# Performance work log

Measured on AMD Instinct MI355X. Metric: run time of the kernel, lower is better.

Reference implementation:

```python
import jax, jax.numpy as jnp
import numpy as np

EPS = 1e-13


def _masked_softmax(logits, mask_last):
    # logits: [B, Q, K]; mask_last: [B, 1, K] float {0,1}
    # Faithful to torch source: multiply logits by mask (NOT additive -inf),
    # softmax, re-mask, renormalize.
    p = jax.nn.softmax(logits * mask_last, axis=-1) * mask_last
    return p / (jnp.sum(p, axis=-1, keepdims=True) + EPS)


def setup_inputs() -> dict:
    key = jax.random.key(0)
    k1, k2, k3, k4 = jax.random.split(key, 4)
    B, LA, LB, H = 16, 1024, 1024, 512
    premise_batch = jax.random.normal(k1, (B, LA, H), dtype=jnp.float32)
    hypothesis_batch = jax.random.normal(k2, (B, LB, H), dtype=jnp.float32)
    premise_mask = jax.random.randint(k3, (B, LA), 0, 2).astype(jnp.float32)
    hypothesis_mask = jax.random.randint(k4, (B, LB), 0, 2).astype(jnp.float32)
    # avoid fully-masked rows (degenerate)
    premise_mask = premise_mask.at[:, 0].set(1.0)
    hypothesis_mask = hypothesis_mask.at[:, 0].set(1.0)
    return {
        "premise_batch": premise_batch,
        "premise_mask": premise_mask,
        "hypothesis_batch": hypothesis_batch,
        "hypothesis_mask": hypothesis_mask,
    }


def reference(premise_batch, premise_mask, hypothesis_batch, hypothesis_mask):
    # sim[b,i,j] = <a_i, b_j>
    sim = jnp.einsum("bih,bjh->bij", premise_batch, hypothesis_batch)
    prem_hyp_attn = _masked_softmax(sim, hypothesis_mask[:, None, :])           # [B,LA,LB]
    hyp_prem_attn = _masked_softmax(sim.transpose(0, 2, 1), premise_mask[:, None, :])  # [B,LB,LA]
    attended_premises = jnp.einsum("bij,bjh->bih", prem_hyp_attn, hypothesis_batch)
    attended_premises = attended_premises * premise_mask[:, :, None]
    attended_hypotheses = jnp.einsum("bji,bjh->bih", hyp_prem_attn.transpose(0, 2, 1), premise_batch)
    attended_hypotheses = attended_hypotheses * hypothesis_mask[:, :, None]
    return (attended_premises, attended_hypotheses)
```

## Files before the change

### kernel.cpp

```cpp
#include <hip/hip_runtime.h>
#include <hip/hip_fp16.h>
#include <math.h>

#define NB   16
#define SLA  1024
#define SLB  1024
#define HH   512

typedef __attribute__((ext_vector_type(4))) float  f32x4;
typedef __attribute__((ext_vector_type(8))) short  s16x8;
typedef __attribute__((ext_vector_type(4))) int    i32x4;

#define QS    (6.5f / 127.f)
#define QINVS (127.f / 6.5f)

__device__ __forceinline__ unsigned short f2bf(float x){
  unsigned u = __float_as_uint(x);
  u += 0x7fffu + ((u >> 16) & 1u);
  return (unsigned short)(u >> 16);
}
__device__ __forceinline__ float bf2f(unsigned short h){
  return __uint_as_float(((unsigned)h) << 16);
}
__device__ __forceinline__ float h2f(unsigned short h){
  return __half2float(__ushort_as_half(h));
}
__device__ __forceinline__ unsigned fkey(float f){
  unsigned u = __float_as_uint(f);
  return ((int)u < 0) ? ~u : (u | 0x80000000u);
}
__device__ __forceinline__ float funkey(unsigned k){
  return __uint_as_float((k & 0x80000000u) ? (k & 0x7fffffffu) : ~k);
}

__device__ __forceinline__ void gl2lds16(const void* g, void* l){
  __builtin_amdgcn_global_load_lds(
      (__attribute__((address_space(1))) unsigned int*)(unsigned long long)(size_t)g,
      (__attribute__((address_space(3))) unsigned int*)(unsigned int)(size_t)l,
      16, 0, 0);
}

__global__ __launch_bounds__(256) void scan_kernel(
    const float* __restrict__ pmask, const float* __restrict__ hmask,
    int* __restrict__ pIdx, int* __restrict__ hIdx,
    int* __restrict__ pCnt, int* __restrict__ hCnt,
    int* __restrict__ pPad, int* __restrict__ hPad,
    unsigned* __restrict__ rowMaxU, unsigned* __restrict__ colMaxU)
{
  __shared__ int ps[256];
  const int b     = blockIdx.x;
  const int which = blockIdx.y;
  const int t     = threadIdx.x;
  const float* m = (which ? hmask : pmask) + b * 1024;
  int* idx = (which ? hIdx : pIdx) + b * 1024;
  int* cnt = which ? hCnt : pCnt;
  int* pad = which ? hPad : pPad;

  #pragma unroll
  for (int v = 0; v < 4; ++v){
    int g = b * 1024 + t + v * 256;
    if (which == 0){
      rowMaxU[g] = 0u;
    } else {
      colMaxU[g] = 0u;
    }
  }

  int f[4], s = 0;
  #pragma unroll
  for (int e = 0; e < 4; ++e){
    f[e] = m[t * 4 + e] > 0.5f ? 1 : 0;
    s += f[e];
  }
  ps[t] = s;
  __syncthreads();
  for (int off = 1; off < 256; off <<= 1){
    int v = (t >= off) ? ps[t - off] : 0;
    __syncthreads();
    ps[t] += v;
    __syncthreads();
  }
  int pos = ps[t] - s;
  #pragma unroll
  for (int e = 0; e < 4; ++e){
    if (f[e]) idx[pos++] = t * 4 + e;
  }
  if (t == 0){
    int total = ps[255];
    cnt[b] = total;
    pad[b] = (total + 127) & ~127;
  }
}

__global__ __launch_bounds__(256) void zero_out_kernel(
    const float* __restrict__ pmask, const float* __restrict__ hmask,
    float* __restrict__ out)
{
  const int r = blockIdx.x * 4 + (threadIdx.x >> 6);
  const int side = r >> 14;
  const int b    = (r >> 10) & 15;
  const int row  = r & 1023;
  const float mv = (side ? hmask : pmask)[b * 1024 + row];
  if (mv > 0.5f) return;
  float4 z = {0.f, 0.f, 0.f, 0.f};
  float* p = out + (size_t)side * NB * SLA * HH
                 + ((size_t)b * 1024 + row) * 512 + (threadIdx.x & 63) * 8;
  *(float4*)p = z;
  *(float4*)(p + 4) = z;
}

__global__ __launch_bounds__(256) void cvt_gather_kernel(
    const float* __restrict__ prem, const float* __restrict__ hyp,
    const int* __restrict__ pIdx, const int* __restrict__ hIdx,
    const int* __restrict__ pCnt, const int* __restrict__ hCnt,
    const int* __restrict__ pPad, const int* __restrict__ hPad,
    char* __restrict__ premD1, char* __restrict__ premD0,
    char* __restrict__ hypD1,  char* __restrict__ hypD0,
    unsigned short* __restrict__ PremT, unsigned short* __restrict__ HypT)
{
  __shared__ unsigned short tv[64][72];
  __shared__ int sIdx[64];

  const int tensor = blockIdx.z >> 4;
  const int b  = blockIdx.z & 15;
  const int l0 = blockIdx.y * 64;
  const int h0 = blockIdx.x * 64;
  const int t  = threadIdx.x;

  const int cnt = tensor ? hCnt[b] : pCnt[b];
  const int pad = tensor ? hPad[b] : pPad[b];
  if (l0 >= pad) return;

  const float* X = tensor ? hyp : prem;
  const int* idx = (tensor ? hIdx : pIdx) + b * 1024;
  char* D1 = tensor ? hypD1 : premD1;
  char* D0 = tensor ? hypD0 : premD0;
  unsigned short* XT = tensor ? HypT : PremT;

  if (t < 64){
    int jc = l0 + t;
    sIdx[t] = (jc < cnt) ? idx[jc] : -1;
  }
  __syncthreads();

  #pragma unroll
  for (int it = 0; it < 4; ++it){
    int r = (t >> 4) + it * 16;
    int c = (t & 15) * 4;
    int orig = sIdx[r];
    float4 x = {0.f, 0.f, 0.f, 0.f};
    if (orig >= 0)
      x = *(const float4*)(X + ((size_t)b * 1024 + orig) * HH + h0 + c);
    float xv[4] = {x.x, x.y, x.z, x.w};
    char d1v[4], d0v[4];
    #pragma unroll
    for (int e = 0; e < 4; ++e){
      float xs = xv[e] * QINVS;
      float x1 = rintf(xs);
      x1 = fminf(127.f, fmaxf(-127.f, x1));
      float x0 = rintf((xs - x1) * 256.f);
      x0 = fminf(127.f, fmaxf(-128.f, x0));
      d1v[e] = (char)(int)x1;
      d0v[e] = (char)(int)x0;
      tv[c + e][r] = f2bf(xv[e]);
    }
    size_t go = ((size_t)b * 1024 + l0 + r) * HH + h0 + c;
    *(char4*)(D1 + go) = make_char4(d1v[0], d1v[1], d1v[2], d1v[3]);
    *(char4*)(D0 + go) = make_char4(d0v[0], d0v[1], d0v[2], d0v[3]);
  }
  __syncthreads();
  const int w   = t >> 2;
  const int seg = (t & 3) * 16;
  const uint4* src = (const uint4*)&tv[w][seg];
  uint4* dst = (uint4*)(XT + ((size_t)b * HH + h0 + w) * 1024 + l0 + seg);
  dst[0] = src[0];
  dst[1] = src[1];
}

__global__ __launch_bounds__(256, 3) void sim_gemm_v6_kernel(
    const char* __restrict__ premD1, const char* __restrict__ premD0,
    const char* __restrict__ hypD1,  const char* __restrict__ hypD0,
    const int* __restrict__ pCnt, const int* __restrict__ hCnt,
    const int* __restrict__ pPad, const int* __restrict__ hPad,
    unsigned short* __restrict__ simH, unsigned short* __restrict__ simT,
    unsigned* __restrict__ rowMaxU, unsigned* __restrict__ colMaxU)
{
  union __align__(16) Smem {
    struct {
      char A1[128 * 64];
      char A0[128 * 64];
      char B1[64 * 64];
      char B0[64 * 64];
    } g;
    unsigned short tp[64][136];
  };
  __shared__ Smem su;
#define sA1 (su.g.A1)
#define sA0 (su.g.A0)
#define sB1 (su.g.B1)
#define sB0 (su.g.B0)

  const int b  = blockIdx.z;
  const int i0 = blockIdx.y * 128;
  const int j0 = blockIdx.x * 64;
  const int t  = threadIdx.x;

  const int pc = pCnt[b], hc = hCnt[b];
  if (i0 >= pPad[b] || j0 >= hPad[b]) return;

  const char* A1 = premD1 + ((size_t)b * 1024 + i0) * HH;
  const char* A0 = premD0 + ((size_t)b * 1024 + i0) * HH;
  const char* B1 = hypD1  + ((size_t)b * 1024 + j0) * HH;
  const char* B0 = hypD0  + ((size_t)b * 1024 + j0) * HH;

  const int sr = t >> 2;
  const int gc = ((t & 3) ^ (sr & 3)) * 16;
  const int lco = (t & 3) * 16;

  const int lane = t & 63;
  const int wr = (t >> 7) & 1;
  const int wc = (t >> 6) & 1;
  const int q  = lane >> 4;
  const int ln = lane & 15;
  const int fo = (q ^ (ln & 3)) * 16;

  i32x4 acc1[4][2], accc[4][2];
  #pragma unroll
  for (int mt = 0; mt < 4; ++mt)
    #pragma unroll
    for (int nt = 0; nt < 2; ++nt){
      acc1[mt][nt] = (i32x4){0, 0, 0, 0};
      accc[mt][nt] = (i32x4){0, 0, 0, 0};
    }

  for (int k0 = 0; k0 < HH; k0 += 64){
    __syncthreads();
    {
      const size_t goA = (size_t)sr * HH + k0 + gc;
      gl2lds16(A1 + goA, &sA1[sr * 64 + lco]);
      gl2lds16(A0 + goA, &sA0[sr * 64 + lco]);
      const size_t goA2 = (size_t)(64 + sr) * HH + k0 + gc;
      gl2lds16(A1 + goA2, &sA1[(64 + sr) * 64 + lco]);
      gl2lds16(A0 + goA2, &sA0[(64 + sr) * 64 + lco]);
      gl2lds16(B1 + goA, &sB1[sr * 64 + lco]);
      gl2lds16(B0 + goA, &sB0[sr * 64 + lco]);
    }
    __syncthreads();

    i32x4 af[4], bf1[2], bf0[2];
    #pragma unroll
    for (int mt = 0; mt < 4; ++mt)
      af[mt] = *(const i32x4*)&sA1[(wr * 64 + mt * 16 + ln) * 64 + fo];
    #pragma unroll
    for (int nt = 0; nt < 2; ++nt)
      bf1[nt] = *(const i32x4*)&sB1[(wc * 32 + nt * 16 + ln) * 64 + fo];
    #pragma unroll
    for (int mt = 0; mt < 4; ++mt)
      #pragma unroll
      for (int nt = 0; nt < 2; ++nt)
        acc1[mt][nt] = __builtin_amdgcn_mfma_i32_16x16x64_i8(af[mt], bf1[nt], acc1[mt][nt], 0, 0, 0);
    #pragma unroll
    for (int nt = 0; nt < 2; ++nt)
      bf0[nt] = *(const i32x4*)&sB0[(wc * 32 + nt * 16 + ln) * 64 + fo];
    #pragma unroll
    for (int mt = 0; mt < 4; ++mt)
      #pragma unroll
      for (int nt = 0; nt < 2; ++nt)
        accc[mt][nt] = __builtin_amdgcn_mfma_i32_16x16x64_i8(af[mt], bf0[nt], accc[mt][nt], 0, 0, 0);
    #pragma unroll
    for (int mt = 0; mt < 4; ++mt)
      af[mt] = *(const i32x4*)&sA0[(wr * 64 + mt * 16 + ln) * 64 + fo];
    #pragma unroll
    for (int mt = 0; mt < 4; ++mt)
      #pragma unroll
      for (int nt = 0; nt < 2; ++nt)
        accc[mt][nt] = __builtin_amdgcn_mfma_i32_16x16x64_i8(af[mt], bf1[nt], accc[mt][nt], 0, 0, 0);
  }

  const float S2 = QS * QS;
  unsigned short* simb = simH + ((size_t)b * SLA + i0) * SLB + j0;

  float rmx[16];
  #pragma unroll
  for (int e = 0; e < 16; ++e) rmx[e] = -1e30f;
  float cmx[2];
  cmx[0] = -1e30f; cmx[1] = -1e30f;

  __syncthreads();

  #pragma unroll
  for (int mt = 0; mt < 4; ++mt){
    #pragma unroll
    for (int nt = 0; nt < 2; ++nt){
      int col = wc * 32 + nt * 16 + ln;
      bool colv = (j0 + col) < hc;
      unsigned short hv[4];
      #pragma unroll
      for (int rr = 0; rr < 4; ++rr){
        int row = wr * 64 + mt * 16 + q * 4 + rr;
        float f = S2 * ((float)acc1[mt][nt][rr] + (float)accc[mt][nt][rr] * 0.00390625f);
        unsigned short hb = __half_as_ushort(__float2half(f));
        simb[(size_t)row * SLB + col] = hb;
        hv[rr] = hb;
        rmx[mt * 4 + rr] = fmaxf(rmx[mt * 4 + rr], colv ? f : -1e30f);
        cmx[nt] = fmaxf(cmx[nt], (i0 + row) < pc ? f : -1e30f);
      }
      uint2 w;
      w.x = (unsigned)hv[0] | ((unsigned)hv[1] << 16);
      w.y = (unsigned)hv[2] | ((unsigned)hv[3] << 16);
      *(uint2*)&su.tp[col][wr * 64 + mt * 16 + q * 4] = w;
    }
  }
  __syncthreads();
  {
    const int jr  = t >> 2;
    const int seg = (t & 3) * 32;
    const uint4* src = (const uint4*)&su.tp[jr][seg];
    uint4* dst = (uint4*)(simT + ((size_t)b * SLB + j0 + jr) * SLA + i0 + seg);
    dst[0] = src[0];
    dst[1] = src[1];
    dst[2] = src[2];
    dst[3] = src[3];
  }

  #pragma unroll
  for (int e = 0; e < 16; ++e){
    float v = rmx[e];
    v = fmaxf(v, __shfl_xor(v, 1));
    v = fmaxf(v, __shfl_xor(v, 2));
    v = fmaxf(v, __shfl_xor(v, 4));
    v = fmaxf(v, __shfl_xor(v, 8));
    if (ln == 0){
      int row = wr * 64 + (e >> 2) * 16 + q * 4 + (e & 3);
      if (i0 + row < pc)
        atomicMax(rowMaxU + b * 1024 + i0 + row, fkey(v));
    }
  }
  #pragma unroll
  for (int nt = 0; nt < 2; ++nt){
    float v = cmx[nt];
    v = fmaxf(v, __shfl_xor(v, 16));
    v = fmaxf(v, __shfl_xor(v, 32));
    if (q == 0){
      int col = wc * 32 + nt * 16 + ln;
      if (j0 + col < hc)
        atomicMax(colMaxU + b * 1024 + j0 + col, fkey(v));
    }
  }
#undef sA1
#undef sA0
#undef sB1
#undef sB0
}

__global__ __launch_bounds__(256, 4) void av4_kernel(
    const unsigned short* __restrict__ simH,
    const unsigned short* __restrict__ simT,
    const unsigned short* __restrict__ HypT, const unsigned short* __restrict__ PremT,
    const unsigned* __restrict__ rowMaxU, const unsigned* __restrict__ colMaxU,
    const int* __restrict__ pIdx, const int* __restrict__ hIdx,
    const int* __restrict__ pCnt, const int* __restrict__ hCnt,
    const int* __restrict__ pPad, const int* __restrict__ hPad,
    float* __restrict__ out)
{
  __shared__ unsigned short sA[128 * 64];
  __shared__ unsigned short sB[128 * 64];
  __shared__ float sRM[128];
  __shared__ float sScale[128];
  __shared__ int   sIdx[128];

  const int side = blockIdx.z >> 4;
  const int b    = blockIdx.z & 15;
  const int m0   = blockIdx.y * 128;
  const int n0   = blockIdx.x * 128;
  const int t    = threadIdx.x;

  const int cnt  = side ? hCnt[b] : pCnt[b];
  const int mpad = side ? hPad[b] : pPad[b];
  const int kpad = side ? pPad[b] : hPad[b];
  const int kcnt = side ? pCnt[b] : hCnt[b];
  if (m0 >= mpad) return;

  const int* idx = (side ? hIdx : pIdx) + b * 1024;
  float* o = out + (size_t)side * NB * SLA * HH + (size_t)b * 1024 * 512;

  if (t < 128){
    sIdx[t] = idx[m0 + t];
    sRM[t]  = funkey((side ? colMaxU : rowMaxU)[b * 1024 + m0 + t]);
  }

  const int wv = t >> 6;
  const int L  = t & 63;
  const int lr = L >> 3;
  const int sw = L & 7;
  const int gkc = (sw ^ lr) * 8;

  const int ar  = t >> 1;
  const int akh = (t & 1) * 32;

  const int lane = t & 63;
  const int wr = (t >> 7) & 1;
  const int wc = (t >> 6) & 1;
  const int q  = lane >> 4;
  const int ln = lane & 15;
  const int fsw = ln & 7;

  const unsigned short* As = (side ? simT : simH) + (size_t)b * 1024 * 1024;
  const unsigned short* Bt = (side ? PremT : HypT) + (size_t)b * 512 * 1024;
  const unsigned short* Arow = As + (size_t)(m0 + ar) * 1024 + akh;

  uint4 aP0 = *(const uint4*)(Arow + 0);
  uint4 aP1 = *(const uint4*)(Arow + 8);
  uint4 aP2 = *(const uint4*)(Arow + 16);
  uint4 aP3 = *(const uint4*)(Arow + 24);

  __syncthreads();
  const float rm = sRM[ar];

  float rs = 0.f;

  f32x4 acc[4][4];
  #pragma unroll
  for (int mt = 0; mt < 4; ++mt)
    #pragma unroll
    for (int nt = 0; nt < 4; ++nt)
      acc[mt][nt] = (f32x4){0.f, 0.f, 0.f, 0.f};

  for (int k0 = 0; k0 < kpad; k0 += 64){
    __syncthreads();
    #pragma unroll
    for (int s = 0; s < 4; ++s){
      int row = wv * 32 + s * 8 + lr;
      gl2lds16(Bt + (size_t)(n0 + row) * 1024 + k0 + gkc, &sB[row * 64 + sw * 8]);
    }
    uint4 aN0, aN1, aN2, aN3;
    if (k0 + 64 < kpad){
      const unsigned short* sp = Arow + k0 + 64;
      aN0 = *(const uint4*)(sp + 0);
      aN1 = *(const uint4*)(sp + 8);
      aN2 = *(const uint4*)(sp + 16);
      aN3 = *(const uint4*)(sp + 24);
    }
    {
      uint4 ua[4] = {aP0, aP1, aP2, aP3};
      const bool full = (k0 + 64 <= kcnt);
      #pragma unroll
      for (int cc = 0; cc < 4; ++cc){
        uint4 u = ua[cc];
        unsigned uw[4] = {u.x, u.y, u.z, u.w};
        unsigned short pb[8];
        if (full){
          #pragma unroll
          for (int d = 0; d < 4; ++d){
            float v0 = h2f((unsigned short)(uw[d] & 0xffff));
            float v1 = h2f((unsigned short)(uw[d] >> 16));
            float p0 = __expf(v0 - rm);
            float p1 = __expf(v1 - rm);
            rs += p0 + p1;
            pb[d * 2]     = f2bf(p0);
            pb[d * 2 + 1] = f2bf(p1);
          }
        } else {
          int kb = k0 + akh + cc * 8;
          #pragma unroll
          for (int d = 0; d < 4; ++d){
            float v0 = h2f((unsigned short)(uw[d] & 0xffff));
            float v1 = h2f((unsigned short)(uw[d] >> 16));
            float p0 = (kb + d * 2 + 0) < kcnt ? __expf(v0 - rm) : 0.f;
            float p1 = (kb + d * 2 + 1) < kcnt ? __expf(v1 - rm) : 0.f;
            rs += p0 + p1;
            pb[d * 2]     = f2bf(p0);
            pb[d * 2 + 1] = f2bf(p1);
          }
        }
        uint4 w;
        w.x = (unsigned)pb[0] | ((unsigned)pb[1] << 16);
        w.y = (unsigned)pb[2] | ((unsigned)pb[3] << 16);
        w.z = (unsigned)pb[4] | ((unsigned)pb[5] << 16);
        w.w = (unsigned)pb[6] | ((unsigned)pb[7] << 16);
        int c   = (t & 1) * 4 + cc;
        int pos = c ^ (ar & 7);
        *(uint4*)&sA[ar * 64 + pos * 8] = w;
      }
    }
    __syncthreads();

    #pragma unroll
    for (int h = 0; h < 2; ++h){
      s16x8 af[4], bfr[4];
      #pragma unroll
      for (int mt = 0; mt < 4; ++mt){
        int r = wr * 64 + mt * 16 + ln;
        af[mt] = *(const s16x8*)&sA[r * 64 + (((h << 2) + q) ^ fsw) * 8];
      }
      #pragma unroll
      for (int nt = 0; nt < 4; ++nt){
        int r = wc * 64 + nt * 16 + ln;
        bfr[nt] = *(const s16x8*)&sB[r * 64 + (((h << 2) + q) ^ fsw) * 8];
      }
      #pragma unroll
      for (int mt = 0; mt < 4; ++mt)
        #pragma unroll
        for (int nt = 0; nt < 4; ++nt)
          acc[mt][nt] = __builtin_amdgcn_mfma_f32_16x16x32_bf16(af[mt], bfr[nt], acc[mt][nt], 0, 0, 0);
    }

    aP0 = aN0; aP1 = aN1; aP2 = aN2; aP3 = aN3;
  }

  rs += __shfl_xor(rs, 1);
  __syncthreads();
  if ((t & 1) == 0) sScale[ar] = 1.f / rs;
  __syncthreads();

  #pragma unroll
  for (int mt = 0; mt < 4; ++mt)
    #pragma unroll
    for (int nt = 0; nt < 4; ++nt){
      int col = n0 + wc * 64 + nt * 16 + ln;
      #pragma unroll
      for (int rr = 0; rr < 4; ++rr){
        int rowL = wr * 64 + mt * 16 + q * 4 + rr;
        if (m0 + rowL < cnt)
          o[(size_t)sIdx[rowL] * 512 + col] = acc[mt][nt][rr] * sScale[rowL];
      }
    }
}

extern "C" void kernel_launch(void* const* d_in, const int* in_sizes, int n_in,
                              void* d_out, int out_size, void* d_ws, size_t ws_size,
                              hipStream_t stream)
{
  const float* prem  = (const float*)d_in[0];
  const float* pmask = (const float*)d_in[1];
  const float* hyp   = (const float*)d_in[2];
  const float* hmask = (const float*)d_in[3];
  float* out = (float*)d_out;

  char* ws = (char*)d_ws;
  unsigned short* simH = (unsigned short*)(ws);
  unsigned short* simT = (unsigned short*)(ws + 33554432);
  unsigned* rowMaxU = (unsigned*)(ws + 67108864);
  unsigned* colMaxU = (unsigned*)(ws + 67108864 + 2 * 65536);
  int* pIdx = (int*)(ws + 67108864 + 4 * 65536);
  int* hIdx = (int*)(ws + 67108864 + 5 * 65536);
  int* pCnt = (int*)(ws + 67108864 + 6 * 65536);
  int* hCnt = (int*)(ws + 67108864 + 6 * 65536 + 256);
  int* pPad = (int*)(ws + 67108864 + 6 * 65536 + 512);
  int* hPad = (int*)(ws + 67108864 + 6 * 65536 + 768);
  const size_t base2 = 67108864 + 4 * 65536 + 1048576;
  char* premD1 = (char*)(ws + base2);
  char* premD0 = (char*)(ws + base2 + 8388608);
  char* hypD1  = (char*)(ws + base2 + 16777216);
  char* hypD0  = (char*)(ws + base2 + 25165824);
  unsigned short* PremT = (unsigned short*)(ws + base2 + 33554432);
  unsigned short* HypT  = (unsigned short*)(ws + base2 + 50331648);
  const size_t need = base2 + 100663296;
  if (ws_size < need) return;

  scan_kernel<<<dim3(16, 2), 256, 0, stream>>>(pmask, hmask, pIdx, hIdx,
                                               pCnt, hCnt, pPad, hPad,
                                               rowMaxU, colMaxU);
  zero_out_kernel<<<dim3(8192), 256, 0, stream>>>(pmask, hmask, out);
  cvt_gather_kernel<<<dim3(8, 16, 32), 256, 0, stream>>>(
      prem, hyp, pIdx, hIdx, pCnt, hCnt, pPad, hPad,
      premD1, premD0, hypD1, hypD0, PremT, HypT);
  sim_gemm_v6_kernel<<<dim3(16, 8, NB), 256, 0, stream>>>(
      premD1, premD0, hypD1, hypD0, pCnt, hCnt, pPad, hPad,
      simH, simT, rowMaxU, colMaxU);
  av4_kernel<<<dim3(4, 8, 32), 256, 0, stream>>>(
      simH, simT, HypT, PremT, rowMaxU, colMaxU,
      pIdx, hIdx, pCnt, hCnt, pPad, hPad, out);
}
```

Before: 218.9 us.

## Double-buffer LDS tiles in attention-value GEMM to overlap loads with MFMA

Converts the av kernel's single-buffered A and B shared-memory tiles into ping-pong buffers, so the next chunk's global-to-LDS load and its exp/bf16 packing run after the current chunk's MFMAs, with one barrier per iteration instead of two. The row max is now read straight from global memory rather than staged through shared memory. The cost is double the LDS footprint and launch bounds lowered from 4 to 2 blocks per CU, which may reduce occupancy and latency hiding across blocks.

```diff
diff --git a/kernel.cpp b/kernel.cpp
--- a/kernel.cpp
+++ b/kernel.cpp
@@ -353,7 +353,7 @@
 #undef sB0
 }
 
-__global__ __launch_bounds__(256, 4) void av4_kernel(
+__global__ __launch_bounds__(256, 2) void av5_kernel(
     const unsigned short* __restrict__ simH,
     const unsigned short* __restrict__ simT,
     const unsigned short* __restrict__ HypT, const unsigned short* __restrict__ PremT,
@@ -363,9 +363,8 @@
     const int* __restrict__ pPad, const int* __restrict__ hPad,
     float* __restrict__ out)
 {
-  __shared__ unsigned short sA[128 * 64];
-  __shared__ unsigned short sB[128 * 64];
-  __shared__ float sRM[128];
+  __shared__ unsigned short sA[2][128 * 64];
+  __shared__ unsigned short sB[2][128 * 64];
   __shared__ float sScale[128];
   __shared__ int   sIdx[128];
 
@@ -384,10 +383,7 @@
   const int* idx = (side ? hIdx : pIdx) + b * 1024;
   float* o = out + (size_t)side * NB * SLA * HH + (size_t)b * 1024 * 512;
 
-  if (t < 128){
-    sIdx[t] = idx[m0 + t];
-    sRM[t]  = funkey((side ? colMaxU : rowMaxU)[b * 1024 + m0 + t]);
-  }
+  if (t < 128) sIdx[t] = idx[m0 + t];
 
   const int wv = t >> 6;
   const int L  = t & 63;
@@ -409,15 +405,61 @@
   const unsigned short* Bt = (side ? PremT : HypT) + (size_t)b * 512 * 1024;
   const unsigned short* Arow = As + (size_t)(m0 + ar) * 1024 + akh;
 
-  uint4 aP0 = *(const uint4*)(Arow + 0);
-  uint4 aP1 = *(const uint4*)(Arow + 8);
-  uint4 aP2 = *(const uint4*)(Arow + 16);
-  uint4 aP3 = *(const uint4*)(Arow + 24);
-
-  __syncthreads();
-  const float rm = sRM[ar];
+  const float rm = funkey((side ? colMaxU : rowMaxU)[b * 1024 + m0 + ar]);
 
   float rs = 0.f;
+
+  auto stageB = [&](int ic, int buf){
+    const int k0 = ic * 64;
+    #pragma unroll
+    for (int s = 0; s < 4; ++s){
+      int row = wv * 32 + s * 8 + lr;
+      gl2lds16(Bt + (size_t)(n0 + row) * 1024 + k0 + gkc, &sB[buf][row * 64 + sw * 8]);
+    }
+  };
+  auto expPack = [&](int ic, int buf, uint4 u0, uint4 u1, uint4 u2, uint4 u3){
+    const int k0 = ic * 64;
+    uint4 ua[4] = {u0, u1, u2, u3};
+    const bool full = (k0 + 64 <= kcnt);
+    #pragma unroll
+    for (int cc = 0; cc < 4; ++cc){
+      uint4 u = ua[cc];
+      unsigned uw[4] = {u.x, u.y, u.z, u.w};
+      unsigned short pb[8];
+      if (full){
+        #pragma unroll
+        for (int d = 0; d < 4; ++d){
+          float v0 = h2f((unsigned short)(uw[d] & 0xffff));
+          float v1 = h2f((unsigned short)(uw[d] >> 16));
+          float p0 = __expf(v0 - rm);
+          float p1 = __expf(v1 - rm);
+          rs += p0 + p1;
+          pb[d * 2]     = f2bf(p0);
+          pb[d * 2 + 1] = f2bf(p1);
+        }
+      } else {
+        int kb = k0 + akh + cc * 8;
+        #pragma unroll
+        for (int d = 0; d < 4; ++d){
+          float v0 = h2f((unsigned short)(uw[d] & 0xffff));
+          float v1 = h2f((unsigned short)(uw[d] >> 16));
+          float p0 = (kb + d * 2 + 0) < kcnt ? __expf(v0 - rm) : 0.f;
+          float p1 = (kb + d * 2 + 1) < kcnt ? __expf(v1 - rm) : 0.f;
+          rs += p0 + p1;
+          pb[d * 2]     = f2bf(p0);
+          pb[d * 2 + 1] = f2bf(p1);
+        }
+      }
+      uint4 w;
+      w.x = (unsigned)pb[0] | ((unsigned)pb[1] << 16);
+      w.y = (unsigned)pb[2] | ((unsigned)pb[3] << 16);
+      w.z = (unsigned)pb[4] | ((unsigned)pb[5] << 16);
+      w.w = (unsigned)pb[6] | ((unsigned)pb[7] << 16);
+      int c   = (t & 1) * 4 + cc;
+      int pos = c ^ (ar & 7);
+      *(uint4*)&sA[buf][ar * 64 + pos * 8] = w;
+    }
+  };
 
   f32x4 acc[4][4];
   #pragma unroll
@@ -426,64 +468,31 @@
     for (int nt = 0; nt < 4; ++nt)
       acc[mt][nt] = (f32x4){0.f, 0.f, 0.f, 0.f};
 
-  for (int k0 = 0; k0 < kpad; k0 += 64){
-    __syncthreads();
-    #pragma unroll
-    for (int s = 0; s < 4; ++s){
-      int row = wv * 32 + s * 8 + lr;
-      gl2lds16(Bt + (size_t)(n0 + row) * 1024 + k0 + gkc, &sB[row * 64 + sw * 8]);
-    }
-    uint4 aN0, aN1, aN2, aN3;
-    if (k0 + 64 < kpad){
-      const unsigned short* sp = Arow + k0 + 64;
-      aN0 = *(const uint4*)(sp + 0);
-      aN1 = *(const uint4*)(sp + 8);
-      aN2 = *(const uint4*)(sp + 16);
-      aN3 = *(const uint4*)(sp + 24);
-    }
-    {
-      uint4 ua[4] = {aP0, aP1, aP2, aP3};
-      const bool full = (k0 + 64 <= kcnt);
-      #pragma unroll
-      for (int cc = 0; cc < 4; ++cc){
-        uint4 u = ua[cc];
-        unsigned uw[4] = {u.x, u.y, u.z, u.w};
-        unsigned short pb[8];
-        if (full){
-          #pragma unroll
-          for (int d = 0; d < 4; ++d){
-            float v0 = h2f((unsigned short)(uw[d] & 0xffff));
-            float v1 = h2f((unsigned short)(uw[d] >> 16));
-            float p0 = __expf(v0 - rm);
-            float p1 = __expf(v1 - rm);
-            rs += p0 + p1;
-            pb[d * 2]     = f2bf(p0);
-            pb[d * 2 + 1] = f2bf(p1);
-          }
-        } else {
-          int kb = k0 + akh + cc * 8;
-          #pragma unroll
-          for (int d = 0; d < 4; ++d){
-            float v0 = h2f((unsigned short)(uw[d] & 0xffff));
-            float v1 = h2f((unsigned short)(uw[d] >> 16));
-            float p0 = (kb + d * 2 + 0) < kcnt ? __expf(v0 - rm) : 0.f;
-            float p1 = (kb + d * 2 + 1) < kcnt ? __expf(v1 - rm) : 0.f;
-            rs += p0 + p1;
-            pb[d * 2]     = f2bf(p0);
-            pb[d * 2 + 1] = f2bf(p1);
-          }
-        }
-        uint4 w;
-        w.x = (unsigned)pb[0] | ((unsigned)pb[1] << 16);
-        w.y = (unsigned)pb[2] | ((unsigned)pb[3] << 16);
-        w.z = (unsigned)pb[4] | ((unsigned)pb[5] << 16);
-        w.w = (unsigned)pb[6] | ((unsigned)pb[7] << 16);
-        int c   = (t & 1) * 4 + cc;
-        int pos = c ^ (ar & 7);
-        *(uint4*)&sA[ar * 64 + pos * 8] = w;
-      }
-    }
-    __syncthreads();
+  const int nch = kpad >> 6;
+
+  stageB(0, 0);
+  {
+    uint4 a0 = *(const uint4*)(Arow + 0);
+    uint4 a1 = *(const uint4*)(Arow + 8);
+    uint4 a2 = *(const uint4*)(Arow + 16);
+    uint4 a3 = *(const uint4*)(Arow + 24);
+    expPack(0, 0, a0, a1, a2, a3);
+  }
+  __syncthreads();
+
+  int cur = 0;
+  for (int ic = 0; ic < nch; ++ic){
+    const int nxtc = ic + 1;
+    const int nxt  = cur ^ 1;
+    uint4 a0, a1, a2, a3;
+    if (nxtc < nch){
+      stageB(nxtc, nxt);
+      const unsigned short* sp = Arow + nxtc * 64;
+      a0 = *(const uint4*)(sp + 0);
+      a1 = *(const uint4*)(sp + 8);
+      a2 = *(const uint4*)(sp + 16);
+      a3 = *(const uint4*)(sp + 24);
+    }
 
     #pragma unroll
     for (int h = 0; h < 2; ++h){
@@ -491,12 +500,12 @@
       #pragma unroll
       for (int mt = 0; mt < 4; ++mt){
         int r = wr * 64 + mt * 16 + ln;
-        af[mt] = *(const s16x8*)&sA[r * 64 + (((h << 2) + q) ^ fsw) * 8];
+        af[mt] = *(const s16x8*)&sA[cur][r * 64 + (((h << 2) + q) ^ fsw) * 8];
       }
       #pragma unroll
       for (int nt = 0; nt < 4; ++nt){
         int r = wc * 64 + nt * 16 + ln;
-        bfr[nt] = *(const s16x8*)&sB[r * 64 + (((h << 2) + q) ^ fsw) * 8];
+        bfr[nt] = *(const s16x8*)&sB[cur][r * 64 + (((h << 2) + q) ^ fsw) * 8];
       }
       #pragma unroll
       for (int mt = 0; mt < 4; ++mt)
@@ -505,11 +514,14 @@
           acc[mt][nt] = __builtin_amdgcn_mfma_f32_16x16x32_bf16(af[mt], bfr[nt], acc[mt][nt], 0, 0, 0);
     }
 
-    aP0 = aN0; aP1 = aN1; aP2 = aN2; aP3 = aN3;
+    if (nxtc < nch)
+      expPack(nxtc, nxt, a0, a1, a2, a3);
+
+    __syncthreads();
+    cur = nxt;
   }
 
   rs += __shfl_xor(rs, 1);
-  __syncthreads();
   if ((t & 1) == 0) sScale[ar] = 1.f / rs;
   __syncthreads();
 
@@ -568,7 +580,7 @@
   sim_gemm_v6_kernel<<<dim3(16, 8, NB), 256, 0, stream>>>(
       premD1, premD0, hypD1, hypD0, pCnt, hCnt, pPad, hPad,
       simH, simT, rowMaxU, colMaxU);
-  av4_kernel<<<dim3(4, 8, 32), 256, 0, stream>>>(
+  av5_kernel<<<dim3(4, 8, 32), 256, 0, stream>>>(
       simH, simT, HypT, PremT, rowMaxU, colMaxU,
       pIdx, hIdx, pCnt, hCnt, pPad, hPad, out);
 }
```

After: 220.1 us. No clear change (+0.5%).
